# Optimization experiments

Measured on AMD Instinct MI355X. Metric: run time of the kernel, lower is better.

The kernel has to match this reference:

```python
import jax, jax.numpy as jnp
import numpy as np

B, S, D, H = 4, 4096, 1024, 16
DK = D // H
EPS = 1e-6

def _feature_map(x):
    # ELU + 1 -> strictly positive features
    return jax.nn.elu(x) + 1.0

def setup_inputs() -> dict:
    key = jax.random.key(0)
    ks = jax.random.split(key, 11)
    s = 1.0 / np.sqrt(D)
    return {
        "query": jax.random.normal(ks[0], (B, S, D), jnp.float32),
        "key":   jax.random.normal(ks[1], (B, S, D), jnp.float32),
        "value": jax.random.normal(ks[2], (B, S, D), jnp.float32),
        "Wq": jax.random.uniform(ks[3], (D, D), jnp.float32, -s, s),
        "bq": jax.random.uniform(ks[4], (D,), jnp.float32, -s, s),
        "Wk": jax.random.uniform(ks[5], (D, D), jnp.float32, -s, s),
        "bk": jax.random.uniform(ks[6], (D,), jnp.float32, -s, s),
        "Wv": jax.random.uniform(ks[7], (D, D), jnp.float32, -s, s),
        "bv": jax.random.uniform(ks[8], (D,), jnp.float32, -s, s),
        "Wo": jax.random.uniform(ks[9], (D, D), jnp.float32, -s, s),
        "bo": jax.random.uniform(ks[10], (D,), jnp.float32, -s, s),
    }

def reference(query, key, value, Wq, bq, Wk, bk, Wv, bv, Wo, bo):
    def heads(x, W, b):
        # torch Linear: x @ W.T + b, then split heads -> [B, H, S, DK]
        y = x @ W.T + b
        return y.reshape(B, S, H, DK).transpose(0, 2, 1, 3)

    Q = _feature_map(heads(query, Wq, bq))
    K = _feature_map(heads(key, Wk, bk))
    V = heads(value, Wv, bv)

    # KV[b,h,m,d] = sum_n K[b,h,n,d] * V[b,h,n,m]  (d: K feat dim, m: V dim)
    KV = jnp.einsum('bhnd,bhnm->bhmd', K, V)
    # normalizer Z[b,h,n] = Q[b,h,n,:] . sum_n K
    Z = jnp.einsum('bhnd,bhd->bhn', Q, K.sum(axis=2))[..., None] + EPS
    out = jnp.einsum('bhnd,bhmd->bhnm', Q, KV) / Z  # [B,H,S,DK]
    out = out.transpose(0, 2, 1, 3).reshape(B, S, D)
    return out @ Wo.T + bo
```

## Files before the change

### kernel.cpp

```cpp
#include <hip/hip_runtime.h>
#include <math.h>

#define Bb 4
#define Ss 4096
#define Dd 1024
#define Hh 16
#define DKk 64
#define Mm (Bb * Ss)
#define NCH 16

typedef __attribute__((ext_vector_type(8))) short bf16x8;
typedef __attribute__((ext_vector_type(4))) float f32x4;

__device__ __forceinline__ unsigned short f2bf(float f) {
  unsigned u = __float_as_uint(f);
  u += 0x7FFFu + ((u >> 16) & 1u);
  return (unsigned short)(u >> 16);
}
__device__ __forceinline__ float bf2f(unsigned short s) {
  return __uint_as_float(((unsigned)s) << 16);
}
__device__ __forceinline__ unsigned cvt2(float lo, float hi) {
  unsigned r;
  asm("v_cvt_pk_bf16_f32 %0, %1, %2" : "=v"(r) : "v"(lo), "v"(hi));
  return r;
}

#define GLOAD(dst, src)                                                     \
  __builtin_amdgcn_global_load_lds(                                         \
      (const __attribute__((address_space(1))) void*)(src),                 \
      (__attribute__((address_space(3))) void*)(dst), 16, 0, 0)

__global__ __launch_bounds__(256) void cvt_f32_bf16(
    const float* __restrict__ s0, const float* __restrict__ s1,
    const float* __restrict__ s2, const float* __restrict__ s3,
    unsigned short* __restrict__ d0, unsigned short* __restrict__ d1,
    unsigned short* __restrict__ d2, unsigned short* __restrict__ d3, int n4) {
  const float* s; unsigned short* d;
  switch (blockIdx.y) {
    case 0:  s = s0; d = d0; break;
    case 1:  s = s1; d = d1; break;
    case 2:  s = s2; d = d2; break;
    default: s = s3; d = d3; break;
  }
  const int i = blockIdx.x * 256 + threadIdx.x;
  if (i < n4) {
    float4 v = ((const float4*)s)[i];
    ushort4 o;
    o.x = f2bf(v.x); o.y = f2bf(v.y); o.z = f2bf(v.z); o.w = f2bf(v.w);
    ((ushort4*)d)[i] = o;
  }
}

__global__ __launch_bounds__(256) void cvt_pk_f32_bf16(
    const float* __restrict__ s0, const float* __restrict__ s1,
    unsigned short* __restrict__ d0, unsigned short* __restrict__ d1,
    int n8) {
  const float* s = blockIdx.y ? s1 : s0;
  unsigned short* d = blockIdx.y ? d1 : d0;
  for (long i = (long)blockIdx.x * 256 + threadIdx.x; i < n8;
       i += (long)gridDim.x * 256) {
    float4 a = ((const float4*)s)[2 * i];
    float4 b = ((const float4*)s)[2 * i + 1];
    int4 w;
    w.x = cvt2(a.x, a.y); w.y = cvt2(a.z, a.w);
    w.z = cvt2(b.x, b.y); w.w = cvt2(b.z, b.w);
    ((int4*)d)[i] = w;
  }
}

#define PHASE(mh, nh)                                                        \
  {                                                                          \
    bf16x8 af[4][2], bv_[2][2];                                              \
    _Pragma("unroll") for (int mi = 0; mi < 4; ++mi)                         \
      _Pragma("unroll") for (int ks = 0; ks < 2; ++ks)                       \
        af[mi][ks] = *(const bf16x8*)(bufA +                                 \
            (rowA0 + (mh) * 64 + mi * 16) * 64 + (swz_rd ^ (ks * 32)));      \
    _Pragma("unroll") for (int ni = 0; ni < 2; ++ni)                         \
      _Pragma("unroll") for (int ks = 0; ks < 2; ++ks)                       \
        bv_[ni][ks] = *(const bf16x8*)(bufB +                                \
            (rowB0 + (nh) * 32 + ni * 16) * 64 + (swz_rd ^ (ks * 32)));      \
    __builtin_amdgcn_s_setprio(1);                                           \
    _Pragma("unroll") for (int mi = 0; mi < 4; ++mi)                         \
      _Pragma("unroll") for (int ni = 0; ni < 2; ++ni)                       \
        _Pragma("unroll") for (int ks = 0; ks < 2; ++ks)                     \
          acc[(mh) * 4 + mi][(nh) * 2 + ni] =                                \
              __builtin_amdgcn_mfma_f32_16x16x32_bf16(                       \
                  af[mi][ks], bv_[ni][ks],                                   \
                  acc[(mh) * 4 + mi][(nh) * 2 + ni], 0, 0, 0);               \
    __builtin_amdgcn_s_setprio(0);                                           \
  }

template <typename OutT>
__device__ __forceinline__ void gemm256_body(
    const unsigned short* __restrict__ A,
    const unsigned short* __restrict__ W,
    const float* __restrict__ bias,
    OutT* __restrict__ C, const int act, const int wg_in,
    unsigned short* lds) {
  const int t = threadIdx.x;
  const int wave = t >> 6, lane = t & 63;
  const int wm = wave >> 2, wn = wave & 3;
  const int fr = lane & 15, fq = lane >> 4;

  const int wg = ((wg_in & 7) << 5) | (wg_in >> 3);
  const int bm = wg >> 2, bn = wg & 3;

  f32x4 acc[8][4];
#pragma unroll
  for (int i = 0; i < 8; ++i)
#pragma unroll
    for (int j = 0; j < 4; ++j) acc[i][j] = (f32x4){0.f, 0.f, 0.f, 0.f};

  const int rbase = t >> 3;
  const int swz_st = ((t & 7) ^ ((t >> 3) & 7)) << 3;
  const unsigned short* gA[4];
  const unsigned short* gB[4];
#pragma unroll
  for (int l = 0; l < 4; ++l) {
    const int r = l * 64 + rbase;
    gA[l] = A + (size_t)(bm * 256 + r) * Dd + swz_st;
    gB[l] = W + (size_t)(bn * 256 + r) * Dd + swz_st;
  }
  const int dstoff = wave * 512;

  const int rowA0 = wm * 128 + fr;
  const int rowB0 = wn * 64 + fr;
  const int swz_rd = (fq * 8) ^ ((fr & 7) << 3);

#pragma unroll
  for (int l = 0; l < 4; ++l) {
    GLOAD(lds + l * 4096 + dstoff, gA[l]);
    GLOAD(lds + 16384 + l * 4096 + dstoff, gB[l]);
  }

  for (int tt = 0; tt < 16; ++tt) {
    unsigned short* bufA = lds + (tt & 1) * 32768;
    unsigned short* bufB = bufA + 16384;
    unsigned short* nA = lds + ((tt & 1) ^ 1) * 32768;
    unsigned short* nB = nA + 16384;
    const int kpre = (tt < 15 ? tt + 1 : 15) * 64;

#pragma unroll
    for (int l = 0; l < 4; ++l) GLOAD(nA + l * 4096 + dstoff, gA[l] + kpre);
    asm volatile("s_waitcnt vmcnt(4)" ::: "memory");
    __builtin_amdgcn_s_barrier();
    PHASE(0, 0)
    __builtin_amdgcn_s_barrier();
#pragma unroll
    for (int l = 0; l < 4; ++l) GLOAD(nB + l * 4096 + dstoff, gB[l] + kpre);
    PHASE(0, 1)
    __builtin_amdgcn_s_barrier();
    PHASE(1, 0)
    __builtin_amdgcn_s_barrier();
    PHASE(1, 1)
    __builtin_amdgcn_s_barrier();
  }

  const size_t row0 = (size_t)bm * 256 + wm * 128 + fq * 4;
  const int col0 = bn * 256 + wn * 64 + fr;
#pragma unroll
  for (int mi = 0; mi < 8; ++mi) {
#pragma unroll
    for (int ni = 0; ni < 4; ++ni) {
      const int col = col0 + ni * 16;
      const float bvl = bias[col];
#pragma unroll
      for (int r = 0; r < 4; ++r) {
        const size_t row = row0 + mi * 16 + r;
        float vv = acc[mi][ni][r] + bvl;
        if (act) vv = (vv > 0.f) ? (vv + 1.f) : __expf(vv);
        if constexpr (sizeof(OutT) == 2)
          ((unsigned short*)C)[row * Dd + col] = f2bf(vv);
        else
          ((float*)C)[row * Dd + col] = vv;
      }
    }
  }
}

template <int ACT, typename OutT>
__global__ __launch_bounds__(512, 2) void gemm256(
    const unsigned short* __restrict__ A, const unsigned short* __restrict__ W,
    const float* __restrict__ bias, OutT* __restrict__ C) {
  __shared__ __align__(16) unsigned short lds[2 * 32768];
  gemm256_body<OutT>(A, W, bias, C, ACT,
                     blockIdx.x + gridDim.x * blockIdx.y, lds);
}

__global__ __launch_bounds__(512, 2) void gemm256_kv(
    const unsigned short* __restrict__ A0, const unsigned short* __restrict__ W0,
    const float* __restrict__ b0, unsigned short* __restrict__ C0,
    const unsigned short* __restrict__ A1, const unsigned short* __restrict__ W1,
    const float* __restrict__ b1, unsigned short* __restrict__ C1) {
  __shared__ __align__(16) unsigned short lds[2 * 32768];
  const int wg = blockIdx.x + gridDim.x * blockIdx.y;
  if (blockIdx.z == 0)
    gemm256_body<unsigned short>(A0, W0, b0, C0, 1, wg, lds);
  else
    gemm256_body<unsigned short>(A1, W1, b1, C1, 0, wg, lds);
}

__global__ __launch_bounds__(256) void kv_partial(
    const unsigned short* __restrict__ Kf, const unsigned short* __restrict__ Vf,
    float* __restrict__ part) {
  const int bx = blockIdx.x;
  const int chunk = bx % NCH;
  const int bh = bx / NCH;
  const int h = bh % Hh, b = bh / Hh;
  const int t = threadIdx.x;
  const int tm = t >> 4, td = t & 15;
  __shared__ float sK[8][64];
  __shared__ float sV[8][64];
  float acc[4][4] = {{0.f}};
  float ksr[4] = {0.f, 0.f, 0.f, 0.f};

  const int which = t >> 7;
  const int idx = t & 127;
  const int rr = idx >> 4;
  const int dpos = (idx & 15) << 2;
  const int colbase = h * DKk;
  const int rows = Ss / NCH;

  for (int n0 = 0; n0 < rows; n0 += 8) {
    const int gr = b * Ss + chunk * rows + n0 + rr;
    const unsigned short* src = which ? Vf : Kf;
    ushort4 raw = *(const ushort4*)&src[(size_t)gr * Dd + colbase + dpos];
    __syncthreads();
    float* dst = which ? &sV[rr][dpos] : &sK[rr][dpos];
    dst[0] = bf2f(raw.x); dst[1] = bf2f(raw.y);
    dst[2] = bf2f(raw.z); dst[3] = bf2f(raw.w);
    __syncthreads();
#pragma unroll
    for (int r = 0; r < 8; ++r) {
      float kv[4], vv[4];
#pragma unroll
      for (int j = 0; j < 4; ++j) kv[j] = sK[r][td * 4 + j];
#pragma unroll
      for (int i = 0; i < 4; ++i) vv[i] = sV[r][tm * 4 + i];
#pragma unroll
      for (int i = 0; i < 4; ++i)
#pragma unroll
        for (int j = 0; j < 4; ++j)
          acc[i][j] = fmaf(vv[i], kv[j], acc[i][j]);
      if (tm == 0) {
#pragma unroll
        for (int j = 0; j < 4; ++j) ksr[j] += kv[j];
      }
    }
  }

  float* p = part + (size_t)bx * 4160;
#pragma unroll
  for (int i = 0; i < 4; ++i)
#pragma unroll
    for (int j = 0; j < 4; ++j)
      p[(tm * 4 + i) * 64 + td * 4 + j] = acc[i][j];
  if (tm == 0) {
#pragma unroll
    for (int j = 0; j < 4; ++j) p[4096 + td * 4 + j] = ksr[j];
  }
}

__global__ __launch_bounds__(256) void kv_reduce(
    const float* __restrict__ part, float* __restrict__ KV,
    float* __restrict__ Ksum) {
  const int bh = blockIdx.x;
  for (int e = threadIdx.x; e < 4160; e += 256) {
    float s = 0.f;
#pragma unroll
    for (int c = 0; c < NCH; ++c)
      s += part[((size_t)bh * NCH + c) * 4160 + e];
    if (e < 4096) KV[(size_t)bh * 4096 + e] = s;
    else Ksum[bh * 64 + (e - 4096)] = s;
  }
}

__global__ __launch_bounds__(256) void attn_mfma(
    unsigned short* __restrict__ Qf, const float* __restrict__ KV,
    const float* __restrict__ Ksum) {
  const int bh = blockIdx.x;
  const int h = bh & (Hh - 1), b = bh >> 4;
  const int t = threadIdx.x;
  const int wave = t >> 6, lane = t & 63;
  const int fr = lane & 15, fq = lane >> 4;

  bf16x8 bfrag[4][2];
  const float* kvb = KV + (size_t)bh * 4096;
#pragma unroll
  for (int nj = 0; nj < 4; ++nj)
#pragma unroll
    for (int ks = 0; ks < 2; ++ks) {
      const float* src = kvb + (nj * 16 + fr) * 64 + ks * 32 + fq * 8;
      const float4 lo = *(const float4*)src;
      const float4 hi = *(const float4*)(src + 4);
      bf16x8 f;
      f[0] = (short)f2bf(lo.x); f[1] = (short)f2bf(lo.y);
      f[2] = (short)f2bf(lo.z); f[3] = (short)f2bf(lo.w);
      f[4] = (short)f2bf(hi.x); f[5] = (short)f2bf(hi.y);
      f[6] = (short)f2bf(hi.z); f[7] = (short)f2bf(hi.w);
      bfrag[nj][ks] = f;
    }
  bf16x8 zfrag[2];
#pragma unroll
  for (int ks = 0; ks < 2; ++ks) {
    bf16x8 f = (bf16x8){0, 0, 0, 0, 0, 0, 0, 0};
    if (fr == 0) {
      const float* src = Ksum + bh * 64 + ks * 32 + fq * 8;
      const float4 lo = *(const float4*)src;
      const float4 hi = *(const float4*)(src + 4);
      f[0] = (short)f2bf(lo.x); f[1] = (short)f2bf(lo.y);
      f[2] = (short)f2bf(lo.z); f[3] = (short)f2bf(lo.w);
      f[4] = (short)f2bf(hi.x); f[5] = (short)f2bf(hi.y);
      f[6] = (short)f2bf(hi.z); f[7] = (short)f2bf(hi.w);
    }
    zfrag[ks] = f;
  }

  const size_t row0 = (size_t)b * Ss + (size_t)blockIdx.y * 256 + wave * 64;
  unsigned short* qbase = Qf + row0 * Dd + h * DKk;
  bf16x8 afrag[4][2];
#pragma unroll
  for (int mi = 0; mi < 4; ++mi)
#pragma unroll
    for (int ks = 0; ks < 2; ++ks)
      afrag[mi][ks] =
          *(const bf16x8*)(qbase + (size_t)(mi * 16 + fr) * Dd + ks * 32 + fq * 8);

  f32x4 acc[4][4], zacc[4];
#pragma unroll
  for (int mi = 0; mi < 4; ++mi) {
    zacc[mi] = (f32x4){0.f, 0.f, 0.f, 0.f};
#pragma unroll
    for (int nj = 0; nj < 4; ++nj) acc[mi][nj] = (f32x4){0.f, 0.f, 0.f, 0.f};
  }
#pragma unroll
  for (int mi = 0; mi < 4; ++mi)
#pragma unroll
    for (int ks = 0; ks < 2; ++ks) {
      zacc[mi] = __builtin_amdgcn_mfma_f32_16x16x32_bf16(
          afrag[mi][ks], zfrag[ks], zacc[mi], 0, 0, 0);
#pragma unroll
      for (int nj = 0; nj < 4; ++nj)
        acc[mi][nj] = __builtin_amdgcn_mfma_f32_16x16x32_bf16(
            afrag[mi][ks], bfrag[nj][ks], acc[mi][nj], 0, 0, 0);
    }

#pragma unroll
  for (int mi = 0; mi < 4; ++mi)
#pragma unroll
    for (int r = 0; r < 4; ++r) {
      const float zv = __shfl(zacc[mi][r], lane & 48) + 1e-6f;
      const float rz = 1.0f / zv;
      const size_t ro = (size_t)(mi * 16 + fq * 4 + r) * Dd;
#pragma unroll
      for (int nj = 0; nj < 4; ++nj)
        qbase[ro + nj * 16 + fr] = f2bf(acc[mi][nj][r] * rz);
    }
}

extern "C" void kernel_launch(void* const* d_in, const int* in_sizes, int n_in,
                              void* d_out, int out_size, void* d_ws, size_t ws_size,
                              hipStream_t stream) {
  const float* q  = (const float*)d_in[0];
  const float* k  = (const float*)d_in[1];
  const float* v  = (const float*)d_in[2];
  const float* Wq = (const float*)d_in[3];
  const float* bq = (const float*)d_in[4];
  const float* Wk = (const float*)d_in[5];
  const float* bk = (const float*)d_in[6];
  const float* Wv = (const float*)d_in[7];
  const float* bv = (const float*)d_in[8];
  const float* Wo = (const float*)d_in[9];
  const float* bo = (const float*)d_in[10];
  float* out = (float*)d_out;

  unsigned short* kb  = (unsigned short*)d_ws;
  unsigned short* vb  = kb + (size_t)Mm * Dd;
  unsigned short* Kf  = vb + (size_t)Mm * Dd;
  unsigned short* Vf  = Kf + (size_t)Mm * Dd;
  unsigned short* Wqb = Vf + (size_t)Mm * Dd;
  unsigned short* Wkb = Wqb + (size_t)Dd * Dd;
  unsigned short* Wvb = Wkb + (size_t)Dd * Dd;
  unsigned short* Wob = Wvb + (size_t)Dd * Dd;
  float* KV   = (float*)(Wob + (size_t)Dd * Dd);
  float* Ksum = KV + (size_t)Bb * Hh * DKk * DKk;
  float* part = (float*)kb;

  dim3 gg(Dd / 256, Mm / 256);
  dim3 ggkv(Dd / 256, Mm / 256, 2);
  const int n8 = (Mm * Dd) / 8;

  cvt_f32_bf16<<<dim3(1024, 4), 256, 0, stream>>>(Wq, Wk, Wv, Wo, Wqb, Wkb, Wvb, Wob,
                                                  (Dd * Dd) / 4);
  cvt_pk_f32_bf16<<<dim3(2048, 2), 256, 0, stream>>>(k, v, kb, vb, n8);
  gemm256_kv<<<ggkv, 512, 0, stream>>>(kb, Wkb, bk, Kf, vb, Wvb, bv, Vf);
  kv_partial<<<Bb * Hh * NCH, 256, 0, stream>>>(Kf, Vf, part);
  kv_reduce<<<Bb * Hh, 256, 0, stream>>>(part, KV, Ksum);
  cvt_pk_f32_bf16<<<dim3(2048, 1), 256, 0, stream>>>(q, nullptr, kb, nullptr, n8);
  gemm256<1, unsigned short><<<gg, 512, 0, stream>>>(kb, Wqb, bq, Kf);
  attn_mfma<<<dim3(Bb * Hh, Ss / 256), 256, 0, stream>>>(Kf, KV, Ksum);
  gemm256<0, float><<<gg, 512, 0, stream>>>(Kf, Wob, bo, out);
}
```

Before: 289.8 us.

## Reorder GEMM LDS tile layout so prefetch is split and interleaved per phase

```diff
diff --git a/kernel.cpp b/kernel.cpp
--- a/kernel.cpp
+++ b/kernel.cpp
@@ -69,27 +69,31 @@
   }
 }
 
-#define PHASE(mh, nh)                                                        \
-  {                                                                          \
-    bf16x8 af[4][2], bv_[2][2];                                              \
-    _Pragma("unroll") for (int mi = 0; mi < 4; ++mi)                         \
-      _Pragma("unroll") for (int ks = 0; ks < 2; ++ks)                       \
-        af[mi][ks] = *(const bf16x8*)(bufA +                                 \
-            (rowA0 + (mh) * 64 + mi * 16) * 64 + (swz_rd ^ (ks * 32)));      \
+#define LOADQ(mh, nh)                                                        \
+  _Pragma("unroll") for (int mi = 0; mi < 4; ++mi)                           \
+    _Pragma("unroll") for (int ks = 0; ks < 2; ++ks)                         \
+      af[mi][ks] = *(const bf16x8*)(bufA +                                   \
+          ((mh) * 128 + wm * 64 + mi * 16 + fr) * 64 + (swz_rd ^ (ks * 32)));\
+  _Pragma("unroll") for (int ni = 0; ni < 2; ++ni)                           \
+    _Pragma("unroll") for (int ks = 0; ks < 2; ++ks)                         \
+      bv_[ni][ks] = *(const bf16x8*)(bufB +                                  \
+          ((nh) * 128 + wn * 32 + ni * 16 + fr) * 64 + (swz_rd ^ (ks * 32)));
+
+#define MFMAQ(mh, nh)                                                        \
+  __builtin_amdgcn_s_setprio(1);                                             \
+  _Pragma("unroll") for (int mi = 0; mi < 4; ++mi)                           \
     _Pragma("unroll") for (int ni = 0; ni < 2; ++ni)                         \
       _Pragma("unroll") for (int ks = 0; ks < 2; ++ks)                       \
-        bv_[ni][ks] = *(const bf16x8*)(bufB +                                \
-            (rowB0 + (nh) * 32 + ni * 16) * 64 + (swz_rd ^ (ks * 32)));      \
-    __builtin_amdgcn_s_setprio(1);                                           \
-    _Pragma("unroll") for (int mi = 0; mi < 4; ++mi)                         \
-      _Pragma("unroll") for (int ni = 0; ni < 2; ++ni)                       \
-        _Pragma("unroll") for (int ks = 0; ks < 2; ++ks)                     \
-          acc[(mh) * 4 + mi][(nh) * 2 + ni] =                                \
-              __builtin_amdgcn_mfma_f32_16x16x32_bf16(                       \
-                  af[mi][ks], bv_[ni][ks],                                   \
-                  acc[(mh) * 4 + mi][(nh) * 2 + ni], 0, 0, 0);               \
-    __builtin_amdgcn_s_setprio(0);                                           \
-  }
+        acc[(mh) * 4 + mi][(nh) * 2 + ni] =                                  \
+            __builtin_amdgcn_mfma_f32_16x16x32_bf16(                         \
+                af[mi][ks], bv_[ni][ks],                                     \
+                acc[(mh) * 4 + mi][(nh) * 2 + ni], 0, 0, 0);                 \
+  __builtin_amdgcn_s_setprio(0);
+
+#define SYNC_PRE_MFMA()                                                      \
+  __builtin_amdgcn_s_barrier();                                              \
+  asm volatile("s_waitcnt lgkmcnt(0)" ::: "memory");                         \
+  __builtin_amdgcn_sched_barrier(0);
 
 template <typename OutT>
 __device__ __forceinline__ void gemm256_body(
@@ -112,27 +116,32 @@
 #pragma unroll
     for (int j = 0; j < 4; ++j) acc[i][j] = (f32x4){0.f, 0.f, 0.f, 0.f};
 
-  const int rbase = t >> 3;
-  const int swz_st = ((t & 7) ^ ((t >> 3) & 7)) << 3;
+  const int r = t >> 3;
+  const int swz_st = ((t & 7) ^ (r & 7)) << 3;
   const unsigned short* gA[4];
   const unsigned short* gB[4];
 #pragma unroll
   for (int l = 0; l < 4; ++l) {
-    const int r = l * 64 + rbase;
-    gA[l] = A + (size_t)(bm * 256 + r) * Dd + swz_st;
-    gB[l] = W + (size_t)(bn * 256 + r) * Dd + swz_st;
+    const int ga_row = (l & 1) * 128 + (l >> 1) * 64 + r;
+    const int bb = l * 2 + (r >> 5);
+    const int gb_row = (bb & 3) * 64 + (bb >> 2) * 32 + (r & 31);
+    gA[l] = A + (size_t)(bm * 256 + ga_row) * Dd + swz_st;
+    gB[l] = W + (size_t)(bn * 256 + gb_row) * Dd + swz_st;
   }
   const int dstoff = wave * 512;
 
-  const int rowA0 = wm * 128 + fr;
-  const int rowB0 = wn * 64 + fr;
   const int swz_rd = (fq * 8) ^ ((fr & 7) << 3);
 
-#pragma unroll
-  for (int l = 0; l < 4; ++l) {
-    GLOAD(lds + l * 4096 + dstoff, gA[l]);
-    GLOAD(lds + 16384 + l * 4096 + dstoff, gB[l]);
-  }
+  GLOAD(lds + 0 * 4096 + dstoff, gA[0]);
+  GLOAD(lds + 1 * 4096 + dstoff, gA[1]);
+  GLOAD(lds + 16384 + 0 * 4096 + dstoff, gB[0]);
+  GLOAD(lds + 16384 + 1 * 4096 + dstoff, gB[1]);
+  GLOAD(lds + 2 * 4096 + dstoff, gA[2]);
+  GLOAD(lds + 3 * 4096 + dstoff, gA[3]);
+  GLOAD(lds + 16384 + 2 * 4096 + dstoff, gB[2]);
+  GLOAD(lds + 16384 + 3 * 4096 + dstoff, gB[3]);
+  asm volatile("s_waitcnt vmcnt(4)" ::: "memory");
+  __builtin_amdgcn_s_barrier();
 
   for (int tt = 0; tt < 16; ++tt) {
     unsigned short* bufA = lds + (tt & 1) * 32768;
@@ -141,34 +150,48 @@
     unsigned short* nB = nA + 16384;
     const int kpre = (tt < 15 ? tt + 1 : 15) * 64;
 
-#pragma unroll
-    for (int l = 0; l < 4; ++l) GLOAD(nA + l * 4096 + dstoff, gA[l] + kpre);
+    bf16x8 af[4][2], bv_[2][2];
+    LOADQ(0, 0)
+    GLOAD(nA + 0 * 4096 + dstoff, gA[0] + kpre);
+    GLOAD(nA + 1 * 4096 + dstoff, gA[1] + kpre);
+    GLOAD(nB + 0 * 4096 + dstoff, gB[0] + kpre);
+    GLOAD(nB + 1 * 4096 + dstoff, gB[1] + kpre);
     asm volatile("s_waitcnt vmcnt(4)" ::: "memory");
+    SYNC_PRE_MFMA()
+    MFMAQ(0, 0)
     __builtin_amdgcn_s_barrier();
-    PHASE(0, 0)
+    LOADQ(0, 1)
+    GLOAD(nA + 2 * 4096 + dstoff, gA[2] + kpre);
+    GLOAD(nA + 3 * 4096 + dstoff, gA[3] + kpre);
+    GLOAD(nB + 2 * 4096 + dstoff, gB[2] + kpre);
+    GLOAD(nB + 3 * 4096 + dstoff, gB[3] + kpre);
+    SYNC_PRE_MFMA()
+    MFMAQ(0, 1)
     __builtin_amdgcn_s_barrier();
-#pragma unroll
-    for (int l = 0; l < 4; ++l) GLOAD(nB + l * 4096 + dstoff, gB[l] + kpre);
-    PHASE(0, 1)
+    LOADQ(1, 0)
+    SYNC_PRE_MFMA()
+    MFMAQ(1, 0)
     __builtin_amdgcn_s_barrier();
-    PHASE(1, 0)
-    __builtin_amdgcn_s_barrier();
-    PHASE(1, 1)
+    LOADQ(1, 1)
+    asm volatile("s_waitcnt vmcnt(4)" ::: "memory");
+    SYNC_PRE_MFMA()
+    MFMAQ(1, 1)
     __builtin_amdgcn_s_barrier();
   }
 
   const size_t row0 = (size_t)bm * 256 + wm * 128 + fq * 4;
   const int col0 = bn * 256 + wn * 64 + fr;
 #pragma unroll
-  for (int mi = 0; mi < 8; ++mi) {
-#pragma unroll
-    for (int ni = 0; ni < 4; ++ni) {
-      const int col = col0 + ni * 16;
+  for (int a = 0; a < 8; ++a) {
+    const size_t row_a = row0 + (a >> 2) * 64 + (a & 3) * 16;
+#pragma unroll
+    for (int b = 0; b < 4; ++b) {
+      const int col = col0 + (b >> 1) * 32 + (b & 1) * 16;
       const float bvl = bias[col];
 #pragma unroll
-      for (int r = 0; r < 4; ++r) {
-        const size_t row = row0 + mi * 16 + r;
-        float vv = acc[mi][ni][r] + bvl;
+      for (int rr2 = 0; rr2 < 4; ++rr2) {
+        const size_t row = row_a + rr2;
+        float vv = acc[a][b][rr2] + bvl;
         if (act) vv = (vv > 0.f) ? (vv + 1.f) : __expf(vv);
         if constexpr (sizeof(OutT) == 2)
           ((unsigned short*)C)[row * Dd + col] = f2bf(vv);
```

Result: no change. 293.9 us (+1.4%).
